# Performance work log

Measured on AMD Instinct MI355X. Metric: run time of the kernel, lower is better.

## Reference

```python
import math
import jax, jax.numpy as jnp
import numpy as np

B, D_MODEL, SEQ_LEN = 8, 1024, 4096
EMB_DIM, ORDER = 3, 64
TARGET, FAST_PCT, SLOW_PCT = 0.01, 0.3, 1.5  # ExponentialModulation defaults


def _pos_emb(L):
    # PositionalEmbedding buffers built for SEQ_LEN, sliced to L
    bands = (EMB_DIM - 1) // 2
    t = jnp.linspace(0.0, 1.0, SEQ_LEN)[None, :, None]                 # [1,S,1]
    t_r = jnp.linspace(0.0, SEQ_LEN - 1.0, SEQ_LEN)[None, :, None]
    w_ang = 2.0 * math.pi * t_r / SEQ_LEN                              # [1,S,1]
    f = jnp.linspace(1e-4, float(bands - 1), bands)[None, None, :]     # [1,1,bands]
    ph = f * w_ang                                                      # [1,S,bands]
    # z = exp(-1j*f*w): real = cos(ph), imag = -sin(ph)
    z = jnp.concatenate([t, jnp.cos(ph), -jnp.sin(ph)], axis=-1)        # [1,S,EMB_DIM]
    return z[:, :L], t[:, :L]


def setup_inputs() -> dict:
    key = jax.random.key(0)
    ks = jax.random.split(key, 9)
    s = 0.2  # small init scale for MLP weights
    return {
        "x": jax.random.normal(ks[0], (B, D_MODEL, SEQ_LEN), jnp.float32),
        "bias_param": jax.random.normal(ks[1], (D_MODEL,), jnp.float32),
        "W1": jax.random.normal(ks[2], (EMB_DIM, ORDER), jnp.float32) * s,
        "b1": jax.random.normal(ks[3], (ORDER,), jnp.float32) * s,
        "W2": jax.random.normal(ks[4], (ORDER, ORDER), jnp.float32) * s,
        "b2": jax.random.normal(ks[5], (ORDER,), jnp.float32) * s,
        "W3": jax.random.normal(ks[6], (ORDER, ORDER), jnp.float32) * s,
        "b3": jax.random.normal(ks[7], (ORDER,), jnp.float32) * s,
        "Wout": jax.random.normal(ks[8], (ORDER, D_MODEL), jnp.float32) * s,
        "freq": jnp.ones((ORDER,), jnp.float32),  # Sin freq, w=1 (shared across all Sin acts)
        "L": SEQ_LEN,
    }


def reference(x, bias_param, W1, b1, W2, b2, W3, b3, Wout, freq, L):
    # ---- implicit filter: k = MLP(pos_emb) * exp_modulation ----
    z, t = _pos_emb(L)                       # [1,L,EMB_DIM], [1,L,1]
    h = jnp.sin(freq * (z @ W1 + b1))        # shared Sin activation
    h = jnp.sin(freq * (h @ W2 + b2))
    h = jnp.sin(freq * (h @ W3 + b3))
    h = h @ Wout                             # [1,L,D]
    max_d = math.log(TARGET) / FAST_PCT
    min_d = math.log(TARGET) / SLOW_PCT
    deltas = jnp.abs(jnp.linspace(min_d, max_d, D_MODEL))[None, None, :]
    k = (h * jnp.exp(-t * deltas))[0].T      # [D,L] per-channel filters
    # ---- FFT long convolution with residual bias path (gelu=False) ----
    N = 2 * L
    u_f = jnp.fft.rfft(x, n=N)               # [B,D,N/2+1]
    k_f = jnp.fft.rfft(k, n=N)               # [D,N/2+1]
    y = jnp.fft.irfft(u_f * k_f, n=N)[..., :L]
    out = y + x * bias_param[:, None]
    return out.astype(x.dtype)
```

## Files before the change

### kernel.cpp

```cpp
#include <hip/hip_runtime.h>
#include <math.h>

#define SEQ    4096
#define NFFT   8192
#define DMODEL 1024
#define ORDER  64
#define CT     512
#define MLPT   256

typedef float2 cf;

#define ZI(c) ((c) ^ ((((c) >> 4) & 7) << 1))

__device__ __forceinline__ cf cadd(cf a, cf b) { return make_float2(a.x + b.x, a.y + b.y); }
__device__ __forceinline__ cf csub(cf a, cf b) { return make_float2(a.x - b.x, a.y - b.y); }
__device__ __forceinline__ cf cmul(cf a, cf b) { return make_float2(a.x * b.x - a.y * b.y, a.x * b.y + a.y * b.x); }
__device__ __forceinline__ cf cmulj(cf a, cf b) { return make_float2(a.x * b.x + a.y * b.y, a.y * b.x - a.x * b.y); }

#define RT2 0.70710678118654752f
#define C16 0.92387953251128676f
#define S16 0.38268343236508977f

template<bool INV>
__device__ __forceinline__ cf cmulc(cf a, float cx, float sy) {
    if (!INV) return make_float2(a.x * cx + a.y * sy, a.y * cx - a.x * sy);
    else      return make_float2(a.x * cx - a.y * sy, a.y * cx + a.x * sy);
}
template<bool INV> __device__ __forceinline__ cf tw8_1(cf d) {
    if (!INV) return make_float2(RT2 * (d.x + d.y), RT2 * (d.y - d.x));
    else      return make_float2(RT2 * (d.x - d.y), RT2 * (d.y + d.x));
}
template<bool INV> __device__ __forceinline__ cf tw8_2(cf d) {
    if (!INV) return make_float2(d.y, -d.x);
    else      return make_float2(-d.y, d.x);
}
template<bool INV> __device__ __forceinline__ cf tw8_3(cf d) {
    if (!INV) return make_float2(RT2 * (d.y - d.x), -RT2 * (d.x + d.y));
    else      return make_float2(-RT2 * (d.x + d.y), RT2 * (d.x - d.y));
}

template<bool INV>
__device__ __forceinline__ void dft4(cf& x0, cf& x1, cf& x2, cf& x3) {
    cf A = cadd(x0, x2), B = csub(x0, x2);
    cf C = cadd(x1, x3), D = csub(x1, x3);
    x0 = cadd(A, C); x2 = csub(A, C);
    if (!INV) { x1 = make_float2(B.x + D.y, B.y - D.x); x3 = make_float2(B.x - D.y, B.y + D.x); }
    else      { x1 = make_float2(B.x - D.y, B.y + D.x); x3 = make_float2(B.x + D.y, B.y - D.x); }
}

template<bool INV>
__device__ __forceinline__ void dft8(cf v[8]) {
    cf s0 = cadd(v[0], v[4]), s1 = cadd(v[1], v[5]), s2 = cadd(v[2], v[6]), s3 = cadd(v[3], v[7]);
    cf d0 = csub(v[0], v[4]), d1 = csub(v[1], v[5]), d2 = csub(v[2], v[6]), d3 = csub(v[3], v[7]);
    cf t1 = tw8_1<INV>(d1), t2 = tw8_2<INV>(d2), t3 = tw8_3<INV>(d3);
    dft4<INV>(s0, s1, s2, s3);
    dft4<INV>(d0, t1, t2, t3);
    v[0] = s0; v[2] = s1; v[4] = s2; v[6] = s3;
    v[1] = d0; v[3] = t1; v[5] = t2; v[7] = t3;
}

template<bool INV>
__device__ __forceinline__ void dft16(cf v[16]) {
    cf s[8], t[8];
    #pragma unroll
    for (int m = 0; m < 8; m++) { s[m] = cadd(v[m], v[m + 8]); t[m] = csub(v[m], v[m + 8]); }
    t[1] = cmulc<INV>(t[1], C16, S16);
    t[2] = tw8_1<INV>(t[2]);
    t[3] = cmulc<INV>(t[3], S16, C16);
    t[4] = tw8_2<INV>(t[4]);
    t[5] = cmulc<INV>(t[5], -S16, C16);
    t[6] = tw8_3<INV>(t[6]);
    t[7] = cmulc<INV>(t[7], -C16, S16);
    dft8<INV>(s); dft8<INV>(t);
    #pragma unroll
    for (int k = 0; k < 8; k++) { v[2 * k] = s[k]; v[2 * k + 1] = t[k]; }
}

template<int L, int S, bool FIRST>
__device__ __forceinline__ void stage_fwd(float2* z, const cf* __restrict__ tw) {
    int t = threadIdx.x;
    int j0 = 2 * (t & (L / 2 - 1));
    int base = (t / (L / 2)) * (8 * L);
    int c0 = base + j0;
    cf a[8], b[8];
    #pragma unroll
    for (int k = 0; k < 8; k++) {
        if (FIRST && k >= 4) { a[k] = make_float2(0.f, 0.f); b[k] = a[k]; }
        else {
            float4 p = *(const float4*)&z[ZI(c0 + k * L)];
            a[k] = make_float2(p.x, p.y); b[k] = make_float2(p.z, p.w);
        }
    }
    dft8<false>(a); dft8<false>(b);
    cf wA1 = tw[S * j0],       wB1 = tw[S * j0 + S];
    cf wA2 = cmul(wA1, wA1),   wB2 = cmul(wB1, wB1);
    cf wA3 = cmul(wA2, wA1),   wB3 = cmul(wB2, wB1);
    cf wA4 = cmul(wA2, wA2),   wB4 = cmul(wB2, wB2);
    cf wA5 = cmul(wA3, wA2),   wB5 = cmul(wB3, wB2);
    cf wA6 = cmul(wA3, wA3),   wB6 = cmul(wB3, wB3);
    cf wA7 = cmul(wA4, wA3),   wB7 = cmul(wB4, wB3);
    a[1] = cmul(a[1], wA1); b[1] = cmul(b[1], wB1);
    a[2] = cmul(a[2], wA2); b[2] = cmul(b[2], wB2);
    a[3] = cmul(a[3], wA3); b[3] = cmul(b[3], wB3);
    a[4] = cmul(a[4], wA4); b[4] = cmul(b[4], wB4);
    a[5] = cmul(a[5], wA5); b[5] = cmul(b[5], wB5);
    a[6] = cmul(a[6], wA6); b[6] = cmul(b[6], wB6);
    a[7] = cmul(a[7], wA7); b[7] = cmul(b[7], wB7);
    #pragma unroll
    for (int k = 0; k < 8; k++)
        *(float4*)&z[ZI(c0 + k * L)] = make_float4(a[k].x, a[k].y, b[k].x, b[k].y);
    __syncthreads();
}

template<int L, int S>
__device__ __forceinline__ void stage_inv(float2* z, const cf* __restrict__ tw) {
    int t = threadIdx.x;
    int j0 = 2 * (t & (L / 2 - 1));
    int base = (t / (L / 2)) * (8 * L);
    int c0 = base + j0;
    cf a[8], b[8];
    #pragma unroll
    for (int k = 0; k < 8; k++) {
        float4 p = *(const float4*)&z[ZI(c0 + k * L)];
        a[k] = make_float2(p.x, p.y); b[k] = make_float2(p.z, p.w);
    }
    cf wA1 = tw[S * j0],       wB1 = tw[S * j0 + S];
    cf wA2 = cmul(wA1, wA1),   wB2 = cmul(wB1, wB1);
    cf wA3 = cmul(wA2, wA1),   wB3 = cmul(wB2, wB1);
    cf wA4 = cmul(wA2, wA2),   wB4 = cmul(wB2, wB2);
    cf wA5 = cmul(wA3, wA2),   wB5 = cmul(wB3, wB2);
    cf wA6 = cmul(wA3, wA3),   wB6 = cmul(wB3, wB3);
    cf wA7 = cmul(wA4, wA3),   wB7 = cmul(wB4, wB3);
    a[1] = cmulj(a[1], wA1); b[1] = cmulj(b[1], wB1);
    a[2] = cmulj(a[2], wA2); b[2] = cmulj(b[2], wB2);
    a[3] = cmulj(a[3], wA3); b[3] = cmulj(b[3], wB3);
    a[4] = cmulj(a[4], wA4); b[4] = cmulj(b[4], wB4);
    a[5] = cmulj(a[5], wA5); b[5] = cmulj(b[5], wB5);
    a[6] = cmulj(a[6], wA6); b[6] = cmulj(b[6], wB6);
    a[7] = cmulj(a[7], wA7); b[7] = cmulj(b[7], wB7);
    dft8<true>(a); dft8<true>(b);
    #pragma unroll
    for (int k = 0; k < 8; k++)
        *(float4*)&z[ZI(c0 + k * L)] = make_float4(a[k].x, a[k].y, b[k].x, b[k].y);
    __syncthreads();
}

__device__ __forceinline__ int REV3(int u) {
    return ((u & 7) << 6) | (u & 56) | ((u >> 6) & 7);
}

__global__ void mlp_kernel(const float* __restrict__ W1, const float* __restrict__ b1,
                           const float* __restrict__ W2, const float* __restrict__ b2,
                           const float* __restrict__ W3, const float* __restrict__ b3,
                           const float* __restrict__ freq, float* __restrict__ Ht,
                           cf* __restrict__ tw) {
    if (blockIdx.x < NFFT / MLPT) {
        int j = blockIdx.x * MLPT + threadIdx.x;
        double ang = (2.0 * M_PI / (double)NFFT) * (double)j;
        tw[j] = make_float2((float)cos(ang), (float)(-sin(ang)));
    }

    int o = threadIdx.x & 63;
    int p = threadIdx.x >> 6;
    int l = blockIdx.x * 4 + p;
    __shared__ float hs[4][ORDER];

    float t   = (float)l / 4095.0f;
    float ang = 1e-4f * (float)(2.0 * M_PI) * (float)l / 4096.0f;
    float z0 = t, z1 = cosf(ang), z2 = -sinf(ang);
    float fo = freq[o];

    float a = z0 * W1[o] + z1 * W1[ORDER + o] + z2 * W1[2 * ORDER + o] + b1[o];
    hs[p][o] = sinf(fo * a);
    __syncthreads();

    a = b2[o];
    #pragma unroll
    for (int i = 0; i < ORDER; i++) a += hs[p][i] * W2[i * ORDER + o];
    float h2 = sinf(fo * a);
    __syncthreads();
    hs[p][o] = h2;
    __syncthreads();

    a = b3[o];
    #pragma unroll
    for (int i = 0; i < ORDER; i++) a += hs[p][i] * W3[i * ORDER + o];
    Ht[o * SEQ + l] = sinf(fo * a);
}

__global__ __launch_bounds__(MLPT) void kgen2_kernel(const float* __restrict__ Wout,
                                                     const float* __restrict__ Ht,
                                                     float* __restrict__ kfil) {
    __shared__ float Hs[ORDER][68];
    __shared__ float Ws[ORDER][68];
    int t  = threadIdx.x;
    int dt = blockIdx.x & 15, lt = blockIdx.x >> 4;

    #pragma unroll
    for (int r = 0; r < 4; r++) {
        int idx = t + 256 * r;
        int o = idx >> 4, c4 = (idx & 15) * 4;
        *(float4*)&Hs[o][c4] = *(const float4*)&Ht[o * SEQ + lt * 64 + c4];
        *(float4*)&Ws[o][c4] = *(const float4*)&Wout[o * DMODEL + dt * 64 + c4];
    }
    __syncthreads();

    int lq = (t & 15) * 4;
    int dq = (t >> 4) * 4;
    float acc[4][4] = {{0.f}};
    #pragma unroll 8
    for (int o = 0; o < ORDER; o++) {
        float4 h = *(float4*)&Hs[o][lq];
        float4 w = *(float4*)&Ws[o][dq];
        acc[0][0] += w.x * h.x; acc[0][1] += w.x * h.y; acc[0][2] += w.x * h.z; acc[0][3] += w.x * h.w;
        acc[1][0] += w.y * h.x; acc[1][1] += w.y * h.y; acc[1][2] += w.y * h.z; acc[1][3] += w.y * h.w;
        acc[2][0] += w.z * h.x; acc[2][1] += w.z * h.y; acc[2][2] += w.z * h.z; acc[2][3] += w.z * h.w;
        acc[3][0] += w.w * h.x; acc[3][1] += w.w * h.y; acc[3][2] += w.w * h.z; acc[3][3] += w.w * h.w;
    }

    const float MIN_D = -3.0701134573253944f;
    const float MAX_D = -15.350567286626971f;
    int l0 = lt * 64 + lq;
    #pragma unroll
    for (int di = 0; di < 4; di++) {
        int d = dt * 64 + dq + di;
        float delta = fabsf(MIN_D + (MAX_D - MIN_D) * (float)d / 1023.0f);
        float4 o4;
        o4.x = acc[di][0] * expf(-((float)(l0 + 0) / 4095.0f) * delta);
        o4.y = acc[di][1] * expf(-((float)(l0 + 1) / 4095.0f) * delta);
        o4.z = acc[di][2] * expf(-((float)(l0 + 2) / 4095.0f) * delta);
        o4.w = acc[di][3] * expf(-((float)(l0 + 3) / 4095.0f) * delta);
        *(float4*)&kfil[(size_t)d * SEQ + l0] = o4;
    }
}

__global__ __launch_bounds__(MLPT) void kfft2_kernel(const float* __restrict__ kfil,
                                                     const cf* __restrict__ tw,
                                                     cf* __restrict__ Kbr) {
    int d = blockIdx.x, t = threadIdx.x;
    __shared__ __align__(16) float2 z2[SEQ];

    const float4* kf4 = (const float4*)(kfil + (size_t)d * SEQ);
    #pragma unroll
    for (int m = 0; m < 4; m++) {
        int s = t + 256 * m;
        *(float4*)&z2[ZI(2 * s)] = kf4[s];
    }
    __syncthreads();

    stage_fwd<512, 2, true>(z2, tw);
    stage_fwd<64, 16, false>(z2, tw);
    stage_fwd<8, 128, false>(z2, tw);

    {
        int c0 = 16 * t;
        cf v[16];
        #pragma unroll
        for (int i = 0; i < 8; i++) {
            float4 p = *(const float4*)&z2[ZI(c0 + 2 * i)];
            v[2 * i] = make_float2(p.x, p.y); v[2 * i + 1] = make_float2(p.z, p.w);
        }
        dft8<false>(v); dft8<false>(v + 8);
        #pragma unroll
        for (int i = 0; i < 8; i++)
            *(float4*)&z2[ZI(c0 + 2 * i)] = make_float4(v[2 * i].x, v[2 * i].y,
                                                        v[2 * i + 1].x, v[2 * i + 1].y);
    }
    __syncthreads();

    const float sc = 1.0f / (float)NFFT;
    cf* Kd = Kbr + (size_t)d * NFFT;
    #pragma unroll
    for (int sub = 0; sub < 2; sub++) {
        int tt = t + 256 * sub;
        int r = REV3(tt);
        cf own[8];
        #pragma unroll
        for (int i = 0; i < 4; i++) {
            float4 p = *(const float4*)&z2[ZI(8 * tt + 2 * i)];
            own[2 * i] = make_float2(p.x, p.y); own[2 * i + 1] = make_float2(p.z, p.w);
        }
        cf kv[16];
        if (r == 0) {
            #pragma unroll
            for (int m = 0; m <= 8; m++) {
                cf Cf = own[m & 7], Cg = own[(8 - m) & 7];
                cf A = make_float2(0.5f * (Cf.x + Cg.x), 0.5f * (Cf.y - Cg.y));
                cf B = make_float2(Cf.x - Cg.x, Cf.y + Cg.y);
                cf W = tw[512 * m];
                cf U = make_float2(0.5f * (W.x * B.x - W.y * B.y),
                                   0.5f * (W.x * B.y + W.y * B.x));
                kv[m & 15] = make_float2(sc * (A.x + U.y), sc * (A.y - U.x));
            }
            #pragma unroll
            for (int i = 9; i < 16; i++)
                kv[i] = make_float2(kv[16 - i].x, -kv[16 - i].y);
        } else {
            int bp = REV3(512 - r);
            cf part[8];
            #pragma unroll
            for (int i = 0; i < 4; i++) {
                float4 p = *(const float4*)&z2[ZI(8 * bp + 2 * i)];
                part[2 * i] = make_float2(p.x, p.y); part[2 * i + 1] = make_float2(p.z, p.w);
            }
            #pragma unroll
            for (int i = 0; i < 8; i++) {
                cf Cf = own[i], Cg = part[7 - i];
                cf A = make_float2(0.5f * (Cf.x + Cg.x), 0.5f * (Cf.y - Cg.y));
                cf B = make_float2(Cf.x - Cg.x, Cf.y + Cg.y);
                cf W = tw[r + 512 * i];
                cf U = make_float2(0.5f * (W.x * B.x - W.y * B.y),
                                   0.5f * (W.x * B.y + W.y * B.x));
                kv[i] = make_float2(sc * (A.x + U.y), sc * (A.y - U.x));
            }
            #pragma unroll
            for (int i = 8; i < 16; i++) {
                cf Cf = part[15 - i], Cg = own[i - 8];
                cf A = make_float2(0.5f * (Cf.x + Cg.x), 0.5f * (Cf.y - Cg.y));
                cf B = make_float2(Cf.x - Cg.x, Cf.y + Cg.y);
                cf W = tw[(512 - r) + 512 * (15 - i)];
                cf U = make_float2(0.5f * (W.x * B.x - W.y * B.y),
                                   0.5f * (W.x * B.y + W.y * B.x));
                kv[i] = make_float2(sc * (A.x + U.y), -sc * (A.y - U.x));
            }
        }
        float4* K4 = (float4*)(Kd + 16 * tt);
        #pragma unroll
        for (int i = 0; i < 8; i++)
            K4[i] = make_float4(kv[2 * i].x, kv[2 * i].y, kv[2 * i + 1].x, kv[2 * i + 1].y);
    }
}

__global__ __launch_bounds__(CT, 4) void conv_kernel(const float* __restrict__ x,
                                                     const float* __restrict__ bias,
                                                     const cf* __restrict__ Kbr,
                                                     const cf* __restrict__ tw,
                                                     float* __restrict__ out) {
    int wg = blockIdx.x;
    int d = wg & (DMODEL - 1);
    int pair = wg >> 10;
    int t = threadIdx.x;

    const float2* xa2 = (const float2*)(x + ((size_t)(2 * pair) * DMODEL + d) * SEQ);
    const float2* xb2 = (const float2*)(x + ((size_t)(2 * pair + 1) * DMODEL + d) * SEQ);

    __shared__ __align__(16) float2 z[NFFT];

    float2 ra[4], rb[4];
    #pragma unroll
    for (int m = 0; m < 4; m++) {
        int s = t + 512 * m;
        ra[m] = xa2[s]; rb[m] = xb2[s];
        *(float4*)&z[ZI(2 * s)] = make_float4(ra[m].x, rb[m].x, ra[m].y, rb[m].y);
    }
    __syncthreads();

    stage_fwd<1024, 1, true>(z, tw);
    stage_fwd<128, 8, false>(z, tw);
    stage_fwd<16, 64, false>(z, tw);

    cf v[16];
    int c0 = 16 * t;
    #pragma unroll
    for (int i = 0; i < 8; i++) {
        float4 p = *(const float4*)&z[ZI(c0 + 2 * i)];
        v[2 * i] = make_float2(p.x, p.y); v[2 * i + 1] = make_float2(p.z, p.w);
    }
    dft16<false>(v);
    const float4* K4 = (const float4*)(Kbr + (size_t)d * NFFT + c0);
    #pragma unroll
    for (int i = 0; i < 8; i++) {
        float4 kk = K4[i];
        v[2 * i]     = cmul(v[2 * i],     make_float2(kk.x, kk.y));
        v[2 * i + 1] = cmul(v[2 * i + 1], make_float2(kk.z, kk.w));
    }
    dft16<true>(v);
    #pragma unroll
    for (int i = 0; i < 8; i++)
        *(float4*)&z[ZI(c0 + 2 * i)] = make_float4(v[2 * i].x, v[2 * i].y,
                                                   v[2 * i + 1].x, v[2 * i + 1].y);
    __syncthreads();

    stage_inv<16, 64>(z, tw);
    stage_inv<128, 8>(z, tw);

    {
        int j0 = 2 * t;
        cf a[8], b[8];
        #pragma unroll
        for (int k = 0; k < 8; k++) {
            float4 p = *(const float4*)&z[ZI(j0 + k * 1024)];
            a[k] = make_float2(p.x, p.y); b[k] = make_float2(p.z, p.w);
        }
        cf wA1 = tw[j0],           wB1 = tw[j0 + 1];
        cf wA2 = cmul(wA1, wA1),   wB2 = cmul(wB1, wB1);
        cf wA3 = cmul(wA2, wA1),   wB3 = cmul(wB2, wB1);
        cf wA4 = cmul(wA2, wA2),   wB4 = cmul(wB2, wB2);
        cf wA5 = cmul(wA3, wA2),   wB5 = cmul(wB3, wB2);
        cf wA6 = cmul(wA3, wA3),   wB6 = cmul(wB3, wB3);
        cf wA7 = cmul(wA4, wA3),   wB7 = cmul(wB4, wB3);
        a[1] = cmulj(a[1], wA1); b[1] = cmulj(b[1], wB1);
        a[2] = cmulj(a[2], wA2); b[2] = cmulj(b[2], wB2);
        a[3] = cmulj(a[3], wA3); b[3] = cmulj(b[3], wB3);
        a[4] = cmulj(a[4], wA4); b[4] = cmulj(b[4], wB4);
        a[5] = cmulj(a[5], wA5); b[5] = cmulj(b[5], wB5);
        a[6] = cmulj(a[6], wA6); b[6] = cmulj(b[6], wB6);
        a[7] = cmulj(a[7], wA7); b[7] = cmulj(b[7], wB7);
        dft8<true>(a); dft8<true>(b);

        float bd = bias[d];
        float2* oa2 = (float2*)(out + ((size_t)(2 * pair) * DMODEL + d) * SEQ);
        float2* ob2 = (float2*)(out + ((size_t)(2 * pair + 1) * DMODEL + d) * SEQ);
        #pragma unroll
        for (int m = 0; m < 4; m++) {
            int s = t + 512 * m;
            oa2[s] = make_float2(a[m].x + bd * ra[m].x, b[m].x + bd * ra[m].y);
            ob2[s] = make_float2(a[m].y + bd * rb[m].x, b[m].y + bd * rb[m].y);
        }
    }
}

extern "C" void kernel_launch(void* const* d_in, const int* in_sizes, int n_in,
                              void* d_out, int out_size, void* d_ws, size_t ws_size,
                              hipStream_t stream) {
    (void)in_sizes; (void)n_in; (void)out_size; (void)ws_size;
    const float* x    = (const float*)d_in[0];
    const float* bias = (const float*)d_in[1];
    const float* W1   = (const float*)d_in[2];
    const float* b1   = (const float*)d_in[3];
    const float* W2   = (const float*)d_in[4];
    const float* b2   = (const float*)d_in[5];
    const float* W3   = (const float*)d_in[6];
    const float* b3   = (const float*)d_in[7];
    const float* Wout = (const float*)d_in[8];
    const float* freq = (const float*)d_in[9];
    float* out = (float*)d_out;

    float* wsf  = (float*)d_ws;
    float* Ht   = wsf;
    cf*    tw   = (cf*)(wsf + 262144);
    float* kfil = wsf + 262144 + 16384;
    cf*    Kbr  = (cf*)(wsf + 262144 + 16384 + 4194304);

    hipLaunchKernelGGL(mlp_kernel, dim3(SEQ / 4), dim3(MLPT), 0, stream,
                       W1, b1, W2, b2, W3, b3, freq, Ht, tw);
    hipLaunchKernelGGL(kgen2_kernel, dim3(1024), dim3(MLPT), 0, stream, Wout, Ht, kfil);
    hipLaunchKernelGGL(kfft2_kernel, dim3(DMODEL), dim3(MLPT), 0, stream, kfil, tw, Kbr);
    hipLaunchKernelGGL(conv_kernel, dim3(DMODEL * 4), dim3(CT), 0, stream,
                       x, bias, Kbr, tw, out);
}
```

Baseline: 236.8 us.

## Restructure conv FFT to one radix-8 butterfly per thread with 1024 threads

The convolution kernel moves from 512 threads, each doing two radix-8 butterflies per stage plus a fused dft16 pair around the spectral multiply, to 1024 threads each doing a single radix-8 butterfly. A radix-2 stage is added before and after the pointwise product with the filter spectrum, and the kfft2 output layout is changed to match. The aim is more parallelism and lower register pressure per thread (launch bounds raised to 8). The cost is more LDS passes and barriers, scalar float2 LDS accesses instead of float4, and scalar global loads and stores of x and out.

```diff
diff --git a/kernel.cpp b/kernel.cpp
--- a/kernel.cpp
+++ b/kernel.cpp
@@ -5,7 +5,7 @@
 #define NFFT   8192
 #define DMODEL 1024
 #define ORDER  64
-#define CT     512
+#define CT     1024
 #define MLPT   256
 
 typedef float2 cf;
@@ -59,24 +59,11 @@
     v[1] = d0; v[3] = t1; v[5] = t2; v[7] = t3;
 }
 
-template<bool INV>
-__device__ __forceinline__ void dft16(cf v[16]) {
-    cf s[8], t[8];
-    #pragma unroll
-    for (int m = 0; m < 8; m++) { s[m] = cadd(v[m], v[m + 8]); t[m] = csub(v[m], v[m + 8]); }
-    t[1] = cmulc<INV>(t[1], C16, S16);
-    t[2] = tw8_1<INV>(t[2]);
-    t[3] = cmulc<INV>(t[3], S16, C16);
-    t[4] = tw8_2<INV>(t[4]);
-    t[5] = cmulc<INV>(t[5], -S16, C16);
-    t[6] = tw8_3<INV>(t[6]);
-    t[7] = cmulc<INV>(t[7], -C16, S16);
-    dft8<INV>(s); dft8<INV>(t);
-    #pragma unroll
-    for (int k = 0; k < 8; k++) { v[2 * k] = s[k]; v[2 * k + 1] = t[k]; }
-}
-
-template<int L, int S, bool FIRST>
+#define TW_CHAIN(w1, w2, w3, w4, w5, w6, w7) \
+    cf w2 = cmul(w1, w1); cf w3 = cmul(w2, w1); cf w4 = cmul(w2, w2); \
+    cf w5 = cmul(w3, w2); cf w6 = cmul(w3, w3); cf w7 = cmul(w4, w3);
+
+template<int L, int S, bool FIRST, int TT>
 __device__ __forceinline__ void stage_fwd(float2* z, const cf* __restrict__ tw) {
     int t = threadIdx.x;
     int j0 = 2 * (t & (L / 2 - 1));
@@ -92,13 +79,9 @@
         }
     }
     dft8<false>(a); dft8<false>(b);
-    cf wA1 = tw[S * j0],       wB1 = tw[S * j0 + S];
-    cf wA2 = cmul(wA1, wA1),   wB2 = cmul(wB1, wB1);
-    cf wA3 = cmul(wA2, wA1),   wB3 = cmul(wB2, wB1);
-    cf wA4 = cmul(wA2, wA2),   wB4 = cmul(wB2, wB2);
-    cf wA5 = cmul(wA3, wA2),   wB5 = cmul(wB3, wB2);
-    cf wA6 = cmul(wA3, wA3),   wB6 = cmul(wB3, wB3);
-    cf wA7 = cmul(wA4, wA3),   wB7 = cmul(wB4, wB3);
+    cf wA1 = tw[S * j0], wB1 = tw[S * j0 + S];
+    TW_CHAIN(wA1, wA2, wA3, wA4, wA5, wA6, wA7)
+    TW_CHAIN(wB1, wB2, wB3, wB4, wB5, wB6, wB7)
     a[1] = cmul(a[1], wA1); b[1] = cmul(b[1], wB1);
     a[2] = cmul(a[2], wA2); b[2] = cmul(b[2], wB2);
     a[3] = cmul(a[3], wA3); b[3] = cmul(b[3], wB3);
@@ -112,36 +95,44 @@
     __syncthreads();
 }
 
+template<int L, int S, bool FIRST>
+__device__ __forceinline__ void cstage_fwd(float2* z, const cf* __restrict__ tw) {
+    int b = threadIdx.x;
+    int j = b & (L - 1);
+    int c0 = (b / L) * (8 * L) + j;
+    cf a[8];
+    #pragma unroll
+    for (int k = 0; k < 8; k++) {
+        if (FIRST && k >= 4) a[k] = make_float2(0.f, 0.f);
+        else                 a[k] = z[ZI(c0 + k * L)];
+    }
+    dft8<false>(a);
+    cf w1 = tw[S * j];
+    TW_CHAIN(w1, w2, w3, w4, w5, w6, w7)
+    a[1] = cmul(a[1], w1); a[2] = cmul(a[2], w2); a[3] = cmul(a[3], w3);
+    a[4] = cmul(a[4], w4); a[5] = cmul(a[5], w5); a[6] = cmul(a[6], w6);
+    a[7] = cmul(a[7], w7);
+    #pragma unroll
+    for (int k = 0; k < 8; k++) z[ZI(c0 + k * L)] = a[k];
+    __syncthreads();
+}
+
 template<int L, int S>
-__device__ __forceinline__ void stage_inv(float2* z, const cf* __restrict__ tw) {
-    int t = threadIdx.x;
-    int j0 = 2 * (t & (L / 2 - 1));
-    int base = (t / (L / 2)) * (8 * L);
-    int c0 = base + j0;
-    cf a[8], b[8];
-    #pragma unroll
-    for (int k = 0; k < 8; k++) {
-        float4 p = *(const float4*)&z[ZI(c0 + k * L)];
-        a[k] = make_float2(p.x, p.y); b[k] = make_float2(p.z, p.w);
-    }
-    cf wA1 = tw[S * j0],       wB1 = tw[S * j0 + S];
-    cf wA2 = cmul(wA1, wA1),   wB2 = cmul(wB1, wB1);
-    cf wA3 = cmul(wA2, wA1),   wB3 = cmul(wB2, wB1);
-    cf wA4 = cmul(wA2, wA2),   wB4 = cmul(wB2, wB2);
-    cf wA5 = cmul(wA3, wA2),   wB5 = cmul(wB3, wB2);
-    cf wA6 = cmul(wA3, wA3),   wB6 = cmul(wB3, wB3);
-    cf wA7 = cmul(wA4, wA3),   wB7 = cmul(wB4, wB3);
-    a[1] = cmulj(a[1], wA1); b[1] = cmulj(b[1], wB1);
-    a[2] = cmulj(a[2], wA2); b[2] = cmulj(b[2], wB2);
-    a[3] = cmulj(a[3], wA3); b[3] = cmulj(b[3], wB3);
-    a[4] = cmulj(a[4], wA4); b[4] = cmulj(b[4], wB4);
-    a[5] = cmulj(a[5], wA5); b[5] = cmulj(b[5], wB5);
-    a[6] = cmulj(a[6], wA6); b[6] = cmulj(b[6], wB6);
-    a[7] = cmulj(a[7], wA7); b[7] = cmulj(b[7], wB7);
-    dft8<true>(a); dft8<true>(b);
-    #pragma unroll
-    for (int k = 0; k < 8; k++)
-        *(float4*)&z[ZI(c0 + k * L)] = make_float4(a[k].x, a[k].y, b[k].x, b[k].y);
+__device__ __forceinline__ void cstage_inv(float2* z, const cf* __restrict__ tw) {
+    int b = threadIdx.x;
+    int j = b & (L - 1);
+    int c0 = (b / L) * (8 * L) + j;
+    cf a[8];
+    #pragma unroll
+    for (int k = 0; k < 8; k++) a[k] = z[ZI(c0 + k * L)];
+    cf w1 = tw[S * j];
+    TW_CHAIN(w1, w2, w3, w4, w5, w6, w7)
+    a[1] = cmulj(a[1], w1); a[2] = cmulj(a[2], w2); a[3] = cmulj(a[3], w3);
+    a[4] = cmulj(a[4], w4); a[5] = cmulj(a[5], w5); a[6] = cmulj(a[6], w6);
+    a[7] = cmulj(a[7], w7);
+    dft8<true>(a);
+    #pragma unroll
+    for (int k = 0; k < 8; k++) z[ZI(c0 + k * L)] = a[k];
     __syncthreads();
 }
 
@@ -248,9 +239,9 @@
     }
     __syncthreads();
 
-    stage_fwd<512, 2, true>(z2, tw);
-    stage_fwd<64, 16, false>(z2, tw);
-    stage_fwd<8, 128, false>(z2, tw);
+    stage_fwd<512, 2, true, 256>(z2, tw);
+    stage_fwd<64, 16, false, 256>(z2, tw);
+    stage_fwd<8, 128, false, 256>(z2, tw);
 
     {
         int c0 = 16 * t;
@@ -326,12 +317,12 @@
         }
         float4* K4 = (float4*)(Kd + 16 * tt);
         #pragma unroll
-        for (int i = 0; i < 8; i++)
-            K4[i] = make_float4(kv[2 * i].x, kv[2 * i].y, kv[2 * i + 1].x, kv[2 * i + 1].y);
-    }
-}
-
-__global__ __launch_bounds__(CT, 4) void conv_kernel(const float* __restrict__ x,
+        for (int j = 0; j < 8; j++)
+            K4[j] = make_float4(kv[j].x, kv[j].y, kv[j + 8].x, kv[j + 8].y);
+    }
+}
+
+__global__ __launch_bounds__(CT, 8) void conv_kernel(const float* __restrict__ x,
                                                      const float* __restrict__ bias,
                                                      const cf* __restrict__ Kbr,
                                                      const cf* __restrict__ tw,
@@ -341,81 +332,65 @@
     int pair = wg >> 10;
     int t = threadIdx.x;
 
-    const float2* xa2 = (const float2*)(x + ((size_t)(2 * pair) * DMODEL + d) * SEQ);
-    const float2* xb2 = (const float2*)(x + ((size_t)(2 * pair + 1) * DMODEL + d) * SEQ);
+    const float* xa = x + ((size_t)(2 * pair) * DMODEL + d) * SEQ;
+    const float* xb = x + ((size_t)(2 * pair + 1) * DMODEL + d) * SEQ;
 
     __shared__ __align__(16) float2 z[NFFT];
 
-    float2 ra[4], rb[4];
+    float xa_[4], xb_[4];
     #pragma unroll
     for (int m = 0; m < 4; m++) {
-        int s = t + 512 * m;
-        ra[m] = xa2[s]; rb[m] = xb2[s];
-        *(float4*)&z[ZI(2 * s)] = make_float4(ra[m].x, rb[m].x, ra[m].y, rb[m].y);
-    }
-    __syncthreads();
-
-    stage_fwd<1024, 1, true>(z, tw);
-    stage_fwd<128, 8, false>(z, tw);
-    stage_fwd<16, 64, false>(z, tw);
-
-    cf v[16];
-    int c0 = 16 * t;
-    #pragma unroll
-    for (int i = 0; i < 8; i++) {
-        float4 p = *(const float4*)&z[ZI(c0 + 2 * i)];
-        v[2 * i] = make_float2(p.x, p.y); v[2 * i + 1] = make_float2(p.z, p.w);
-    }
-    dft16<false>(v);
-    const float4* K4 = (const float4*)(Kbr + (size_t)d * NFFT + c0);
-    #pragma unroll
-    for (int i = 0; i < 8; i++) {
-        float4 kk = K4[i];
-        v[2 * i]     = cmul(v[2 * i],     make_float2(kk.x, kk.y));
-        v[2 * i + 1] = cmul(v[2 * i + 1], make_float2(kk.z, kk.w));
-    }
-    dft16<true>(v);
-    #pragma unroll
-    for (int i = 0; i < 8; i++)
-        *(float4*)&z[ZI(c0 + 2 * i)] = make_float4(v[2 * i].x, v[2 * i].y,
-                                                   v[2 * i + 1].x, v[2 * i + 1].y);
-    __syncthreads();
-
-    stage_inv<16, 64>(z, tw);
-    stage_inv<128, 8>(z, tw);
+        int n = t + 1024 * m;
+        xa_[m] = xa[n]; xb_[m] = xb[n];
+        z[ZI(n)] = make_float2(xa_[m], xb_[m]);
+    }
+    __syncthreads();
+
+    cstage_fwd<1024, 1, true>(z, tw);
+    cstage_fwd<128, 8, false>(z, tw);
+    cstage_fwd<16, 64, false>(z, tw);
+    cstage_fwd<2, 512, false>(z, tw);
 
     {
-        int j0 = 2 * t;
-        cf a[8], b[8];
-        #pragma unroll
-        for (int k = 0; k < 8; k++) {
-            float4 p = *(const float4*)&z[ZI(j0 + k * 1024)];
-            a[k] = make_float2(p.x, p.y); b[k] = make_float2(p.z, p.w);
-        }
-        cf wA1 = tw[j0],           wB1 = tw[j0 + 1];
-        cf wA2 = cmul(wA1, wA1),   wB2 = cmul(wB1, wB1);
-        cf wA3 = cmul(wA2, wA1),   wB3 = cmul(wB2, wB1);
-        cf wA4 = cmul(wA2, wA2),   wB4 = cmul(wB2, wB2);
-        cf wA5 = cmul(wA3, wA2),   wB5 = cmul(wB3, wB2);
-        cf wA6 = cmul(wA3, wA3),   wB6 = cmul(wB3, wB3);
-        cf wA7 = cmul(wA4, wA3),   wB7 = cmul(wB4, wB3);
-        a[1] = cmulj(a[1], wA1); b[1] = cmulj(b[1], wB1);
-        a[2] = cmulj(a[2], wA2); b[2] = cmulj(b[2], wB2);
-        a[3] = cmulj(a[3], wA3); b[3] = cmulj(b[3], wB3);
-        a[4] = cmulj(a[4], wA4); b[4] = cmulj(b[4], wB4);
-        a[5] = cmulj(a[5], wA5); b[5] = cmulj(b[5], wB5);
-        a[6] = cmulj(a[6], wA6); b[6] = cmulj(b[6], wB6);
-        a[7] = cmulj(a[7], wA7); b[7] = cmulj(b[7], wB7);
-        dft8<true>(a); dft8<true>(b);
+        int c0 = 8 * t;
+        const float4* K4 = (const float4*)(Kbr + (size_t)d * NFFT + c0);
+        #pragma unroll
+        for (int p = 0; p < 4; p++) {
+            float4 q = *(const float4*)&z[ZI(c0 + 2 * p)];
+            cf u = make_float2(q.x, q.y), v = make_float2(q.z, q.w);
+            cf s0 = cadd(u, v), s1 = csub(u, v);
+            float4 kk = K4[p];
+            s0 = cmul(s0, make_float2(kk.x, kk.y));
+            s1 = cmul(s1, make_float2(kk.z, kk.w));
+            cf u2 = cadd(s0, s1), v2 = csub(s0, s1);
+            *(float4*)&z[ZI(c0 + 2 * p)] = make_float4(u2.x, u2.y, v2.x, v2.y);
+        }
+    }
+    __syncthreads();
+
+    cstage_inv<2, 512>(z, tw);
+    cstage_inv<16, 64>(z, tw);
+    cstage_inv<128, 8>(z, tw);
+
+    {
+        cf a[8];
+        #pragma unroll
+        for (int k = 0; k < 8; k++) a[k] = z[ZI(t + 1024 * k)];
+        cf w1 = tw[t];
+        TW_CHAIN(w1, w2, w3, w4, w5, w6, w7)
+        a[1] = cmulj(a[1], w1); a[2] = cmulj(a[2], w2); a[3] = cmulj(a[3], w3);
+        a[4] = cmulj(a[4], w4); a[5] = cmulj(a[5], w5); a[6] = cmulj(a[6], w6);
+        a[7] = cmulj(a[7], w7);
+        dft8<true>(a);
 
         float bd = bias[d];
-        float2* oa2 = (float2*)(out + ((size_t)(2 * pair) * DMODEL + d) * SEQ);
-        float2* ob2 = (float2*)(out + ((size_t)(2 * pair + 1) * DMODEL + d) * SEQ);
-        #pragma unroll
-        for (int m = 0; m < 4; m++) {
-            int s = t + 512 * m;
-            oa2[s] = make_float2(a[m].x + bd * ra[m].x, b[m].x + bd * ra[m].y);
-            ob2[s] = make_float2(a[m].y + bd * rb[m].x, b[m].y + bd * rb[m].y);
+        float* oa = out + ((size_t)(2 * pair) * DMODEL + d) * SEQ;
+        float* ob = out + ((size_t)(2 * pair + 1) * DMODEL + d) * SEQ;
+        #pragma unroll
+        for (int k = 0; k < 4; k++) {
+            int n = t + 1024 * k;
+            oa[n] = a[k].x + bd * xa_[k];
+            ob[n] = a[k].y + bd * xb_[k];
         }
     }
 }
```

Result: slower. 374.7 us (+58.2%).
